# Kernel optimization log

Hardware: AMD Instinct MI355X
Metric: run time of the kernel (lower is better)

Reference implementation:

```python
import jax, jax.numpy as jnp
import numpy as np

B = 2            # images
N = 1000         # proposals per image (post_nms_top_n testing)
NUM_CLASSES = 81 # incl background
C = NUM_CLASSES - 1
SCORE_THRESH = 0.05
NMS_THRESH = 0.5
DET_PER_IMG = 100


def setup_inputs() -> dict:
    key = jax.random.key(0)
    k1, k2, k3 = jax.random.split(key, 3)
    class_logits = jax.random.normal(k1, (B * N, NUM_CLASSES), dtype=jnp.float32)
    box_regression = jax.random.normal(k2, (B * N, C * 4), dtype=jnp.float32) * 0.25
    u = jax.random.uniform(k3, (B, N, 4), dtype=jnp.float32)
    cx = u[..., 0] * 700.0 + 50.0
    cy = u[..., 1] * 700.0 + 50.0
    w = u[..., 2] * 200.0 + 20.0
    h = u[..., 3] * 200.0 + 20.0
    proposals = jnp.stack([cx - w / 2, cy - h / 2, cx + w / 2, cy + h / 2], axis=-1)
    return {"class_logits": class_logits, "box_regression": box_regression, "proposals": proposals}


def _decode(rel_codes, boxes):
    # rel_codes: [BN, C*4], boxes: [BN, 4] -> decoded [BN, C, 4]
    rel = rel_codes.reshape(-1, C, 4)
    px = (boxes[:, 0] + boxes[:, 2])[:, None] * 0.5
    py = (boxes[:, 1] + boxes[:, 3])[:, None] * 0.5
    pw = (boxes[:, 2] - boxes[:, 0])[:, None]
    ph = (boxes[:, 3] - boxes[:, 1])[:, None]
    gx = rel[..., 0] * pw + px
    gy = rel[..., 1] * ph + py
    gw = pw * jnp.exp(rel[..., 2])
    gh = ph * jnp.exp(rel[..., 3])
    return jnp.stack([gx - gw * 0.5, gy - gh * 0.5, gx + gw * 0.5, gy + gh * 0.5], axis=-1)


def _pairwise_iou(a, b):
    # a: [N,4], b: [M,4] -> [N,M]
    area_a = (a[:, 2] - a[:, 0]) * (a[:, 3] - a[:, 1])
    area_b = (b[:, 2] - b[:, 0]) * (b[:, 3] - b[:, 1])
    lt = jnp.maximum(a[:, None, :2], b[None, :, :2])
    rb = jnp.minimum(a[:, None, 2:], b[None, :, 2:])
    wh = jnp.clip(rb - lt, 0.0)
    inter = wh[..., 0] * wh[..., 1]
    return inter / (area_a[:, None] + area_b[None, :] - inter)


def _nms_one(boxes, scores):
    # boxes: [N,4], scores: [N] for one (image, class)
    order = jnp.argsort(-scores)
    b = boxes[order]
    s = scores[order]
    iou = _pairwise_iou(b, b)          # [N, N]
    valid = s > SCORE_THRESH

    def step(suppressed, xs):
        iou_row, v, i = xs
        keep_i = v & jnp.logical_not(suppressed[i])
        suppressed = jnp.logical_or(suppressed, keep_i & (iou_row > NMS_THRESH))
        return suppressed, keep_i

    n = boxes.shape[0]
    _, keep = jax.lax.scan(step, jnp.zeros((n,), bool), (iou, valid, jnp.arange(n)))
    rank = jnp.cumsum(keep.astype(jnp.int32))
    keep = keep & (rank <= DET_PER_IMG)   # detections_per_img cap per class
    m = keep.astype(s.dtype)
    return b * m[:, None], s * m


def reference(class_logits, box_regression, proposals):
    # softmax scores, drop background column
    scores_all = jax.nn.softmax(class_logits, axis=-1)              # [B*N, 81]
    decoded = _decode(box_regression, proposals.reshape(-1, 4))     # [B*N, C, 4]
    boxes_c = decoded.reshape(B, N, C, 4).transpose(0, 2, 1, 3)     # [B, C, N, 4]
    scores_c = scores_all[:, 1:].reshape(B, N, C).transpose(0, 2, 1)  # [B, C, N]
    boxes_k, scores_k = jax.vmap(jax.vmap(_nms_one))(boxes_c, scores_c)
    # [B, C, N, 5]: kept boxes (zeroed if suppressed) + kept score, sorted by score per class
    return jnp.concatenate([boxes_k, scores_k[..., None]], axis=-1)
```

## Files before the change

kernel.cpp:

```cpp
#include <hip/hip_runtime.h>

#define BB 2
#define NN 1000
#define NC 81
#define CC 80
#define SCORE_THRESH 0.05f
#define NMS_THRESH 0.5f
#define DET_PER_IMG 100
#define K1_BLOCKS 125

__global__ __launch_bounds__(256) void softmax_zero_kernel(
    const float* __restrict__ logits,
    float* __restrict__ sc,
    float* __restrict__ out) {
    __shared__ __align__(16) float stage[16 * NC];
    __shared__ float s_mx[16], s_inv[16];
    const int tid = threadIdx.x;
    const int blk = blockIdx.x;

    float4* outv = (float4*)out;
    for (int k = blk * 256 + tid; k < BB * CC * NN * 5 / 4; k += K1_BLOCKS * 256)
        outv[k] = make_float4(0.f, 0.f, 0.f, 0.f);

    const int r0 = blk * 16;
    const float4* src = (const float4*)(logits + (size_t)r0 * NC);
    float4* dst = (float4*)stage;
    for (int k = tid; k < 16 * NC / 4; k += 256) dst[k] = src[k];
    __syncthreads();

    if (tid < 16) {
        const float* z = stage + tid * NC;
        float mx = z[0];
        #pragma unroll
        for (int k = 1; k < NC; k++) mx = fmaxf(mx, z[k]);
        float sum = 0.f;
        #pragma unroll
        for (int k = 0; k < NC; k++) sum += expf(z[k] - mx);
        s_mx[tid] = mx;
        s_inv[tid] = 1.f / sum;
    }
    __syncthreads();

    for (int idx = tid; idx < CC * 16; idx += 256) {
        int c = idx >> 4, i = idx & 15;
        int r = r0 + i;
        int b = r / NN, n = r - b * NN;
        sc[((size_t)(b * CC + c)) * NN + n] =
            expf(stage[i * NC + c + 1] - s_mx[i]) * s_inv[i];
    }
}

__global__ __launch_bounds__(256) void nms_task_kernel(
    const float* __restrict__ sc,
    const float* __restrict__ boxreg,
    const float* __restrict__ props,
    float* __restrict__ out) {
    __shared__ float s_vs[NN];
    __shared__ int   s_vn[NN];
    __shared__ int   s_sn[NN];
    __shared__ float s_ss[NN];
    __shared__ float s_x1[NN], s_y1[NN], s_x2[NN], s_y2[NN], s_ar[NN];
    __shared__ int   s_supp[NN];
    __shared__ int   s_kf[NN];
    __shared__ int   s_V;

    const int t = blockIdx.x;
    const int b = t / CC, c = t % CC;
    const int tid = threadIdx.x;
    const int rowbase = b * NN;

    if (tid == 0) s_V = 0;
    __syncthreads();

    if (tid < NN / 4) {
        float4 v = ((const float4*)(sc + (size_t)t * NN))[tid];
        float e[4] = {v.x, v.y, v.z, v.w};
        #pragma unroll
        for (int j = 0; j < 4; j++) {
            if (e[j] > SCORE_THRESH) {
                int i = atomicAdd(&s_V, 1);
                s_vn[i] = tid * 4 + j;
                s_vs[i] = e[j];
            }
        }
    }
    __syncthreads();
    const int V = s_V;

    for (int i = tid; i < V; i += 256) {
        float si = s_vs[i];
        int   ni = s_vn[i];
        int p = 0;
        for (int u = 0; u < V; u++) {
            float su = s_vs[u];
            p += (su > si || (su == si && s_vn[u] < ni)) ? 1 : 0;
        }
        s_sn[p] = ni;
        s_ss[p] = si;
    }
    __syncthreads();

    for (int p = tid; p < V; p += 256) {
        int n = s_sn[p];
        int row = rowbase + n;
        float p0 = props[row * 4 + 0], p1 = props[row * 4 + 1];
        float p2 = props[row * 4 + 2], p3 = props[row * 4 + 3];
        float px = (p0 + p2) * 0.5f, py = (p1 + p3) * 0.5f;
        float pw = p2 - p0, ph = p3 - p1;
        const float* rg = boxreg + (size_t)row * (CC * 4) + c * 4;
        float gx = rg[0] * pw + px;
        float gy = rg[1] * ph + py;
        float gw = pw * expf(rg[2]);
        float gh = ph * expf(rg[3]);
        float x1 = gx - gw * 0.5f, y1 = gy - gh * 0.5f;
        float x2 = gx + gw * 0.5f, y2 = gy + gh * 0.5f;
        s_x1[p] = x1; s_y1[p] = y1; s_x2[p] = x2; s_y2[p] = y2;
        s_ar[p] = (x2 - x1) * (y2 - y1);
    }
    __syncthreads();

    if (V <= 64) {
        if (tid < 64) {
            const int lane = tid;
            const bool act = lane < V;
            float x1j = 0.f, y1j = 0.f, x2j = 0.f, y2j = 0.f, aj = 0.f;
            if (act) {
                x1j = s_x1[lane]; y1j = s_y1[lane];
                x2j = s_x2[lane]; y2j = s_y2[lane]; aj = s_ar[lane];
            }
            unsigned long long suppm = 0ull;
            int mykf = 0, kc = 0;
            for (int i = 0; i < V; ++i) {
                if ((suppm >> i) & 1ull) continue;
                ++kc;
                if (lane == i) mykf = kc;
                float x1i = s_x1[i], y1i = s_y1[i];
                float x2i = s_x2[i], y2i = s_y2[i], ai = s_ar[i];
                float xx = fmaxf(x1i, x1j);
                float yy = fmaxf(y1i, y1j);
                float w = fmaxf(fminf(x2i, x2j) - xx, 0.f);
                float h = fmaxf(fminf(y2i, y2j) - yy, 0.f);
                float inter = w * h;
                float iou = inter / (ai + aj - inter);
                bool sup = act && (lane > i) && (iou > NMS_THRESH);
                suppm |= __ballot(sup);
            }
            if (act) s_kf[lane] = mykf;
        }
        __syncthreads();
    } else {
        for (int p = tid; p < V; p += 256) { s_supp[p] = 0; s_kf[p] = 0; }
        __syncthreads();
        int kc = 0;
        for (int i = 0; i < V; i++) {
            if (s_supp[i]) continue;
            kc++;
            if (tid == 0) s_kf[i] = kc;
            float x1i = s_x1[i], y1i = s_y1[i], x2i = s_x2[i], y2i = s_y2[i];
            float ai = s_ar[i];
            for (int j = i + 1 + tid; j < V; j += 256) {
                float xx = fmaxf(x1i, s_x1[j]);
                float yy = fmaxf(y1i, s_y1[j]);
                float w = fmaxf(fminf(x2i, s_x2[j]) - xx, 0.f);
                float h = fmaxf(fminf(y2i, s_y2[j]) - yy, 0.f);
                float inter = w * h;
                float iou = inter / (ai + s_ar[j] - inter);
                if (iou > NMS_THRESH) s_supp[j] = 1;
            }
            __syncthreads();
        }
        __syncthreads();
    }

    for (int p = tid; p < V; p += 256) {
        int kf = s_kf[p];
        if (kf > 0 && kf <= DET_PER_IMG) {
            size_t o = ((size_t)t * NN + (size_t)p) * 5;
            out[o + 0] = s_x1[p];
            out[o + 1] = s_y1[p];
            out[o + 2] = s_x2[p];
            out[o + 3] = s_y2[p];
            out[o + 4] = s_ss[p];
        }
    }
}

extern "C" void kernel_launch(void* const* d_in, const int* in_sizes, int n_in,
                              void* d_out, int out_size, void* d_ws, size_t ws_size,
                              hipStream_t stream) {
    const float* logits = (const float*)d_in[0];
    const float* boxreg = (const float*)d_in[1];
    const float* props  = (const float*)d_in[2];
    float* out = (float*)d_out;
    float* sc  = (float*)d_ws;

    softmax_zero_kernel<<<K1_BLOCKS, 256, 0, stream>>>(logits, sc, out);
    nms_task_kernel<<<BB * CC, 256, 0, stream>>>(sc, boxreg, props, out);
}
```

Baseline: 76.40 us.

## Run small-V NMS path in a single wavefront with precomputed overlap mask

For tasks with at most 64 valid boxes, the rank sort, box decode, NMS and output write now all run inside one 64-lane wavefront. Wave barriers replace block-wide __syncthreads, and results go straight from registers to global memory. The IoU work is moved out of the serial greedy loop: each lane first builds a 64-bit overlap mask, and the sequential loop then only tests bits and ballots. The large-V path keeps the old block-wide logic, with the suppression-flag reset folded into the decode loop. The other 192 threads in the block sit idle on the small path.

Measured after the change: 76.44 us. Within noise of the previous version (+0.1%).

```diff
diff --git a/kernel.cpp b/kernel.cpp
--- a/kernel.cpp
+++ b/kernel.cpp
@@ -87,53 +87,48 @@
     __syncthreads();
     const int V = s_V;
 
-    for (int i = tid; i < V; i += 256) {
-        float si = s_vs[i];
-        int   ni = s_vn[i];
-        int p = 0;
-        for (int u = 0; u < V; u++) {
-            float su = s_vs[u];
-            p += (su > si || (su == si && s_vn[u] < ni)) ? 1 : 0;
-        }
-        s_sn[p] = ni;
-        s_ss[p] = si;
-    }
-    __syncthreads();
-
-    for (int p = tid; p < V; p += 256) {
-        int n = s_sn[p];
-        int row = rowbase + n;
-        float p0 = props[row * 4 + 0], p1 = props[row * 4 + 1];
-        float p2 = props[row * 4 + 2], p3 = props[row * 4 + 3];
-        float px = (p0 + p2) * 0.5f, py = (p1 + p3) * 0.5f;
-        float pw = p2 - p0, ph = p3 - p1;
-        const float* rg = boxreg + (size_t)row * (CC * 4) + c * 4;
-        float gx = rg[0] * pw + px;
-        float gy = rg[1] * ph + py;
-        float gw = pw * expf(rg[2]);
-        float gh = ph * expf(rg[3]);
-        float x1 = gx - gw * 0.5f, y1 = gy - gh * 0.5f;
-        float x2 = gx + gw * 0.5f, y2 = gy + gh * 0.5f;
-        s_x1[p] = x1; s_y1[p] = y1; s_x2[p] = x2; s_y2[p] = y2;
-        s_ar[p] = (x2 - x1) * (y2 - y1);
-    }
-    __syncthreads();
-
     if (V <= 64) {
         if (tid < 64) {
             const int lane = tid;
             const bool act = lane < V;
-            float x1j = 0.f, y1j = 0.f, x2j = 0.f, y2j = 0.f, aj = 0.f;
+
             if (act) {
-                x1j = s_x1[lane]; y1j = s_y1[lane];
-                x2j = s_x2[lane]; y2j = s_y2[lane]; aj = s_ar[lane];
-            }
-            unsigned long long suppm = 0ull;
-            int mykf = 0, kc = 0;
+                float si = s_vs[lane];
+                int   ni = s_vn[lane];
+                int p = 0;
+                for (int u = 0; u < V; u++) {
+                    float su = s_vs[u];
+                    p += (su > si || (su == si && s_vn[u] < ni)) ? 1 : 0;
+                }
+                s_sn[p] = ni;
+                s_ss[p] = si;
+            }
+            __builtin_amdgcn_wave_barrier();
+
+            float x1j = 0.f, y1j = 0.f, x2j = 0.f, y2j = 0.f, aj = 0.f, scj = 0.f;
+            if (act) {
+                int n = s_sn[lane];
+                scj = s_ss[lane];
+                int row = rowbase + n;
+                float p0 = props[row * 4 + 0], p1 = props[row * 4 + 1];
+                float p2 = props[row * 4 + 2], p3 = props[row * 4 + 3];
+                float px = (p0 + p2) * 0.5f, py = (p1 + p3) * 0.5f;
+                float pw = p2 - p0, ph = p3 - p1;
+                const float* rg = boxreg + (size_t)row * (CC * 4) + c * 4;
+                float gx = rg[0] * pw + px;
+                float gy = rg[1] * ph + py;
+                float gw = pw * expf(rg[2]);
+                float gh = ph * expf(rg[3]);
+                x1j = gx - gw * 0.5f; y1j = gy - gh * 0.5f;
+                x2j = gx + gw * 0.5f; y2j = gy + gh * 0.5f;
+                aj = (x2j - x1j) * (y2j - y1j);
+                s_x1[lane] = x1j; s_y1[lane] = y1j;
+                s_x2[lane] = x2j; s_y2[lane] = y2j; s_ar[lane] = aj;
+            }
+            __builtin_amdgcn_wave_barrier();
+
+            unsigned long long ov = 0ull;
             for (int i = 0; i < V; ++i) {
-                if ((suppm >> i) & 1ull) continue;
-                ++kc;
-                if (lane == i) mykf = kc;
                 float x1i = s_x1[i], y1i = s_y1[i];
                 float x2i = s_x2[i], y2i = s_y2[i], ai = s_ar[i];
                 float xx = fmaxf(x1i, x1j);
@@ -142,15 +137,63 @@
                 float h = fmaxf(fminf(y2i, y2j) - yy, 0.f);
                 float inter = w * h;
                 float iou = inter / (ai + aj - inter);
-                bool sup = act && (lane > i) && (iou > NMS_THRESH);
+                if (act && iou > NMS_THRESH) ov |= (1ull << i);
+            }
+
+            unsigned long long suppm = 0ull;
+            int mykf = 0, kc = 0;
+            for (int i = 0; i < V; ++i) {
+                if ((suppm >> i) & 1ull) continue;
+                ++kc;
+                if (lane == i) mykf = kc;
+                bool sup = act && (lane > i) && ((ov >> i) & 1ull);
                 suppm |= __ballot(sup);
             }
-            if (act) s_kf[lane] = mykf;
+
+            if (act && mykf > 0 && mykf <= DET_PER_IMG) {
+                size_t o = ((size_t)t * NN + (size_t)lane) * 5;
+                out[o + 0] = x1j;
+                out[o + 1] = y1j;
+                out[o + 2] = x2j;
+                out[o + 3] = y2j;
+                out[o + 4] = scj;
+            }
+        }
+    } else {
+        for (int i = tid; i < V; i += 256) {
+            float si = s_vs[i];
+            int   ni = s_vn[i];
+            int p = 0;
+            for (int u = 0; u < V; u++) {
+                float su = s_vs[u];
+                p += (su > si || (su == si && s_vn[u] < ni)) ? 1 : 0;
+            }
+            s_sn[p] = ni;
+            s_ss[p] = si;
         }
         __syncthreads();
-    } else {
-        for (int p = tid; p < V; p += 256) { s_supp[p] = 0; s_kf[p] = 0; }
+
+        for (int p = tid; p < V; p += 256) {
+            int n = s_sn[p];
+            int row = rowbase + n;
+            float p0 = props[row * 4 + 0], p1 = props[row * 4 + 1];
+            float p2 = props[row * 4 + 2], p3 = props[row * 4 + 3];
+            float px = (p0 + p2) * 0.5f, py = (p1 + p3) * 0.5f;
+            float pw = p2 - p0, ph = p3 - p1;
+            const float* rg = boxreg + (size_t)row * (CC * 4) + c * 4;
+            float gx = rg[0] * pw + px;
+            float gy = rg[1] * ph + py;
+            float gw = pw * expf(rg[2]);
+            float gh = ph * expf(rg[3]);
+            float x1 = gx - gw * 0.5f, y1 = gy - gh * 0.5f;
+            float x2 = gx + gw * 0.5f, y2 = gy + gh * 0.5f;
+            s_x1[p] = x1; s_y1[p] = y1; s_x2[p] = x2; s_y2[p] = y2;
+            s_ar[p] = (x2 - x1) * (y2 - y1);
+            s_supp[p] = 0;
+            s_kf[p] = 0;
+        }
         __syncthreads();
+
         int kc = 0;
         for (int i = 0; i < V; i++) {
             if (s_supp[i]) continue;
@@ -170,17 +213,17 @@
             __syncthreads();
         }
         __syncthreads();
-    }
-
-    for (int p = tid; p < V; p += 256) {
-        int kf = s_kf[p];
-        if (kf > 0 && kf <= DET_PER_IMG) {
-            size_t o = ((size_t)t * NN + (size_t)p) * 5;
-            out[o + 0] = s_x1[p];
-            out[o + 1] = s_y1[p];
-            out[o + 2] = s_x2[p];
-            out[o + 3] = s_y2[p];
-            out[o + 4] = s_ss[p];
+
+        for (int p = tid; p < V; p += 256) {
+            int kf = s_kf[p];
+            if (kf > 0 && kf <= DET_PER_IMG) {
+                size_t o = ((size_t)t * NN + (size_t)p) * 5;
+                out[o + 0] = s_x1[p];
+                out[o + 1] = s_y1[p];
+                out[o + 2] = s_x2[p];
+                out[o + 3] = s_y2[p];
+                out[o + 4] = s_ss[p];
+            }
         }
     }
 }
```
